# Optimization experiments

Hardware: AMD Instinct MI355X
Metric: run time of the kernel (lower is better)

The kernel has to match this reference:

```python
import jax, jax.numpy as jnp
import numpy as np

H = 32          # heads
E = 32          # head dim = mdl_channels // heads (must equal heads per module bug)
C = 1024        # mdl_channels == in_channels
MAXP = 128      # max_position_embeddings
EPS = 1e-5


def _layernorm(x, g, b):
    mu = jnp.mean(x, axis=-1, keepdims=True)
    var = jnp.var(x, axis=-1, keepdims=True)
    return (x - mu) * jax.lax.rsqrt(var + EPS) * g + b


def setup_inputs() -> dict:
    key = jax.random.key(0)
    ks = jax.random.split(key, 16)
    s = 0.02
    N, L = 4, 1024
    inp = {
        "x": jax.random.normal(ks[0], (N, L, C), jnp.float32),
        "Wq": jax.random.normal(ks[1], (C, C), jnp.float32) * s,
        "bq": jnp.zeros((C,), jnp.float32),
        "Wk": jax.random.normal(ks[2], (C, C), jnp.float32) * s,
        "bk": jnp.zeros((C,), jnp.float32),
        "Wv": jax.random.normal(ks[3], (C, C), jnp.float32) * s,
        "bv": jnp.zeros((C,), jnp.float32),
        "dist_emb": jax.random.normal(ks[4], (2 * MAXP + 1, E), jnp.float32) * s,
        "ln1_g": jnp.ones((C,), jnp.float32),
        "ln1_b": jnp.zeros((C,), jnp.float32),
        "ln2_g": jnp.ones((C,), jnp.float32),
        "ln2_b": jnp.zeros((C,), jnp.float32),
        "W1": jax.random.normal(ks[5], (C, C), jnp.float32) * s,
        "b1": jnp.zeros((C,), jnp.float32),
        "W2": jax.random.normal(ks[6], (C, C), jnp.float32) * s,
        "b2": jnp.zeros((C,), jnp.float32),
    }
    return inp


def reference(x, Wq, bq, Wk, bk, Wv, bv, dist_emb, ln1_g, ln1_b,
              ln2_g, ln2_b, W1, b1, W2, b2):
    N, L, _ = x.shape
    # QKV projections -> (N, L, H, E)
    q = (x @ Wq + bq).reshape(N, L, H, E)
    k = (x @ Wk + bk).reshape(N, L, H, E)
    v = (x @ Wv + bv).reshape(N, L, H, E)

    temp = 1.0 / np.sqrt(E).astype(np.float32)
    # content scores (N, H, L, S)
    QK = jnp.einsum('nlhe,nshe->nhls', q, k)
    # relative position scores (disentangled attention)
    pos = jnp.arange(L)
    dist = jnp.clip(pos[:, None] - pos[None, :], -MAXP, MAXP) + MAXP  # (L, L)
    pe = dist_emb[dist]                                              # (L, L, E)
    QK = QK + jnp.einsum('nlhe,lse->nhls', q, pe) \
            + jnp.einsum('nshe,lse->nhls', k, pe)
    A = jax.nn.softmax(temp * QK, axis=-1)          # dropout: eval mode (identity)
    t = jnp.einsum('nhls,nshe->nlhe', A, v).reshape(N, L, C)

    h = _layernorm(t + x, ln1_g, ln1_b)             # AddNorm (attention)
    m = jax.nn.relu(h @ W1 + b1) @ W2 + b2          # 2-layer MLP
    out = _layernorm(m + h, ln2_g, ln2_b)           # AddNorm (mlp)
    return jnp.swapaxes(out, 0, 1)                  # 'n f c -> f n c'
```

## Files before the change

kernel.cpp:

```cpp
#include <hip/hip_runtime.h>

#define H_ 32
#define E_ 32
#define C_ 1024
#define L_ 1024
#define N_ 4
#define M_ 4096
#define NH_ 128
#define D_ 257
#define DPAD 272
#define QDP 264
#define TEMP_ 0.17677669529663687f
#define QSCALE_ (TEMP_ * 1.4426950408889634f)

typedef unsigned short u16;
typedef __attribute__((ext_vector_type(8))) short short8;
typedef __attribute__((ext_vector_type(4))) float f32x4;
typedef __attribute__((ext_vector_type(4))) unsigned short u16x4;

__device__ __forceinline__ u16 f2bf(float f) {
  union { float f; unsigned u; } v; v.f = f;
  unsigned r = v.u + 0x7fffu + ((v.u >> 16) & 1u);
  return (u16)(r >> 16);
}
__device__ __forceinline__ float bf2f(u16 h) {
  union { unsigned u; float f; } v; v.u = ((unsigned)h) << 16;
  return v.f;
}
__device__ __forceinline__ f32x4 mfma16(short8 a, short8 b, f32x4 c) {
  return __builtin_amdgcn_mfma_f32_16x16x32_bf16(a, b, c, 0, 0, 0);
}
__device__ __forceinline__ float ex2(float x) {
#if __has_builtin(__builtin_amdgcn_exp2f)
  return __builtin_amdgcn_exp2f(x);
#else
  float r;
  asm("v_exp_f32 %0, %1\n\ts_nop 1" : "=v"(r) : "v"(x));
  return r;
#endif
}
__device__ __forceinline__ void gld16(const u16* g, u16* l) {
  __builtin_amdgcn_global_load_lds(
      (const __attribute__((address_space(1))) unsigned int*)g,
      (__attribute__((address_space(3))) unsigned int*)l, 16, 0, 0);
}

__global__ __launch_bounds__(256) void misc_kernel(
    const float* __restrict__ x, const float* __restrict__ demb,
    const float* __restrict__ bq, const float* __restrict__ bk,
    const float* __restrict__ bv, u16* __restrict__ xb,
    u16* __restrict__ demb_b, float* __restrict__ bqkv) {
  const int b = blockIdx.x, tid = threadIdx.x;
  if (b < 4096) {
    int i = b * 256 + tid;
    f32x4 v = reinterpret_cast<const f32x4*>(x)[i];
    u16x4 o2;
    o2[0] = f2bf(v[0]); o2[1] = f2bf(v[1]); o2[2] = f2bf(v[2]); o2[3] = f2bf(v[3]);
    reinterpret_cast<u16x4*>(xb)[i] = o2;
  } else {
    int i = (b - 4096) * 256 + tid;
    if (i < DPAD * E_) demb_b[i] = (i < D_ * E_) ? f2bf(demb[i]) : (u16)0;
    if (i < C_) { bqkv[i] = bq[i]; bqkv[C_ + i] = bk[i]; bqkv[2 * C_ + i] = bv[i]; }
  }
}

__global__ __launch_bounds__(256) void transpose_w_kernel(
    const float* __restrict__ Wq, const float* __restrict__ Wk,
    const float* __restrict__ Wv, const float* __restrict__ W1,
    const float* __restrict__ W2, u16* __restrict__ out_base) {
  __shared__ float tile[32][33];
  const int z = blockIdx.z;
  const float* in = (z == 0) ? Wq : (z == 1) ? Wk : (z == 2) ? Wv : (z == 3) ? W1 : W2;
  u16* out = out_base + (size_t)z * C_ * C_;
  int j0 = blockIdx.x * 32, c0 = blockIdx.y * 32;
#pragma unroll
  for (int i = 0; i < 4; ++i) {
    int cy = threadIdx.y + i * 8;
    tile[cy][threadIdx.x] = in[(size_t)(c0 + cy) * C_ + j0 + threadIdx.x];
  }
  __syncthreads();
#pragma unroll
  for (int i = 0; i < 4; ++i) {
    int jy = threadIdx.y + i * 8;
    out[(size_t)(j0 + jy) * C_ + c0 + threadIdx.x] = f2bf(tile[threadIdx.x][jy]);
  }
}

template <int EPI>
__global__ __launch_bounds__(256) void gemm128_kernel(
    const u16* __restrict__ A, const u16* __restrict__ Bt, int K,
    const float* __restrict__ bias,
    u16* __restrict__ out0, u16* __restrict__ out1, u16* __restrict__ out2) {
  __shared__ u16 As[128 * 64];
  __shared__ u16 Bs[128 * 64];
  const int bid = blockIdx.x;
  const int m0 = (bid & 31) << 7;
  const int n0 = (bid >> 5) << 7;
  const int tid = threadIdx.x;
  const int w = tid >> 6, lane = tid & 63, lhi = lane >> 4, llo = lane & 15;
  const int wr = w >> 1, wc = w & 1;
  const int w4 = w << 2;
  const int srow = lane >> 3, scol = (lane & 7) << 3;
  f32x4 acc[4][4] = {};
  for (int k0 = 0; k0 < K; k0 += 64) {
#pragma unroll
    for (int j = 0; j < 4; ++j) {
      const int seg = w4 + j;
      const int row = (seg << 3) + srow;
      gld16(&A[(size_t)(m0 + row) * K + k0 + scol], &As[seg << 9]);
      gld16(&Bt[(size_t)(n0 + row) * K + k0 + scol], &Bs[seg << 9]);
    }
    __syncthreads();
#pragma unroll
    for (int kk = 0; kk < 2; ++kk) {
      const int ko = (kk << 5) + lhi * 8;
      short8 af[4], bf[4];
#pragma unroll
      for (int mi = 0; mi < 4; ++mi)
        af[mi] = *reinterpret_cast<const short8*>(&As[(wr * 64 + mi * 16 + llo) * 64 + ko]);
#pragma unroll
      for (int ni = 0; ni < 4; ++ni)
        bf[ni] = *reinterpret_cast<const short8*>(&Bs[(wc * 64 + ni * 16 + llo) * 64 + ko]);
#pragma unroll
      for (int mi = 0; mi < 4; ++mi)
#pragma unroll
        for (int ni = 0; ni < 4; ++ni)
          acc[mi][ni] = mfma16(af[mi], bf[ni], acc[mi][ni]);
    }
    __syncthreads();
  }
#pragma unroll
  for (int mi = 0; mi < 4; ++mi)
#pragma unroll
    for (int ni = 0; ni < 4; ++ni)
#pragma unroll
      for (int r = 0; r < 4; ++r) {
        int row = m0 + wr * 64 + mi * 16 + lhi * 4 + r;
        int col = n0 + wc * 64 + ni * 16 + llo;
        float v = acc[mi][ni][r] + bias[col];
        if constexpr (EPI == 0) {
          int which = col >> 10, jj = col & 1023, h = jj >> 5, e2 = jj & 31;
          int n = row >> 10, l = row & 1023;
          int nh = (n << 5) | h;
          if (which == 0) v *= QSCALE_;
          u16 bvv = f2bf(v);
          if (which == 0)      out0[((size_t)((nh << 10) | l)) * 32 + e2] = bvv;
          else if (which == 1) out1[((size_t)((nh << 10) | l)) * 32 + e2] = bvv;
          else                 out2[(((size_t)(nh * 32 + e2)) << 10) | l] = bvv;
        } else if constexpr (EPI == 1) {
          out0[(size_t)row * C_ + col] = f2bf(fmaxf(v, 0.f));
        } else {
          out0[(size_t)row * C_ + col] = f2bf(v);
        }
      }
}

__global__ __launch_bounds__(256) void qdkd_kernel(
    const u16* __restrict__ src, const u16* __restrict__ demb,
    u16* __restrict__ dst, u16* __restrict__ aux0, u16* __restrict__ aux256) {
  const int wt = blockIdx.x * 4 + (threadIdx.x >> 6);
  const int lane = threadIdx.x & 63, lhi = lane >> 4, llo = lane & 15;
  const int m0 = wt << 4;
  short8 a = *reinterpret_cast<const short8*>(&src[(size_t)(m0 + llo) * E_ + lhi * 8]);
#pragma unroll
  for (int ct = 0; ct < 17; ++ct) {
    int d = ct * 16 + llo;
    short8 b = {0, 0, 0, 0, 0, 0, 0, 0};
    if (d < D_) b = *reinterpret_cast<const short8*>(&demb[d * E_ + lhi * 8]);
    f32x4 c = {};
    c = mfma16(a, b, c);
    if (d < D_) {
#pragma unroll
      for (int r = 0; r < 4; ++r) {
        u16 val = f2bf(c[r] * QSCALE_);
        dst[(size_t)(m0 + lhi * 4 + r) * D_ + d] = val;
        if (d == 0)   aux0[m0 + lhi * 4 + r] = val;
        if (d == 256) aux256[m0 + lhi * 4 + r] = val;
      }
    }
  }
}

__global__ __launch_bounds__(256) void attn_kernel(
    const u16* __restrict__ qw, const u16* __restrict__ kw,
    const u16* __restrict__ vT, const u16* __restrict__ dembp,
    const u16* __restrict__ KDg, const u16* __restrict__ kd0a,
    const u16* __restrict__ kd256a, u16* __restrict__ tb) {
  __shared__ u16 QDs[64 * QDP];
  __shared__ u16 kdc[2 * 1024];
  __shared__ u16 Pbuf[4 * 16 * 40];
  __shared__ float Lred[64];
  const int bid = blockIdx.x;
  const int nh = bid & (NH_ - 1);
  const int l0 = (bid >> 7) << 6;
  const int tid = threadIdx.x;
  const int w = tid >> 6, lane = tid & 63, lhi = lane >> 4, llo = lane & 15;
  const int lw0 = l0 + (w << 4);

  const u16* qb  = qw + (size_t)nh * (L_ * E_);
  const u16* kb  = kw + (size_t)nh * (L_ * E_);
  const u16* vb  = vT + (size_t)nh * (E_ * L_);
  const u16* kdg = KDg + (size_t)nh * ((size_t)L_ * D_);

  {
    const int side = tid >> 7, off = (tid & 127) * 8;
    const u16* srcA = (side ? kd256a : kd0a) + (size_t)nh * L_ + off;
    *reinterpret_cast<short8*>(&kdc[side * 1024 + off]) =
        *reinterpret_cast<const short8*>(srcA);
  }

  const short8 qA = *reinterpret_cast<const short8*>(&qb[(size_t)(lw0 + llo) * E_ + lhi * 8]);

#pragma unroll
  for (int dt = 0; dt < 17; ++dt) {
    short8 db = *reinterpret_cast<const short8*>(&dembp[(dt * 16 + llo) * E_ + lhi * 8]);
    f32x4 qd = {};
    qd = mfma16(qA, db, qd);
    const int qrow = (w << 4) + (lhi << 2);
#pragma unroll
    for (int r = 0; r < 4; ++r)
      QDs[(qrow + r) * QDP + dt * 16 + llo] = f2bf(qd[r]);
  }
  __syncthreads();

  const int qr4 = (w << 4) + (lhi << 2);
  float qdf0[4], qdf256[4];
#pragma unroll
  for (int r = 0; r < 4; ++r) {
    qdf0[r]   = bf2f(QDs[(qr4 + r) * QDP + 0]);
    qdf256[r] = bf2f(QDs[(qr4 + r) * QDP + 256]);
  }

  u16* Pw = &Pbuf[w * 16 * 40];
  f32x4 o0 = {}, o1 = {};
  float lacc[4] = {0.f, 0.f, 0.f, 0.f};

  for (int s0 = 0; s0 < L_; s0 += 32) {
    const int se = s0 + 2 * llo;
    short8 kB0 = *reinterpret_cast<const short8*>(&kb[(size_t)se * E_ + lhi * 8]);
    short8 kB1 = *reinterpret_cast<const short8*>(&kb[(size_t)(se + 1) * E_ + lhi * 8]);
    f32x4 st0 = {}, st1 = {};
    st0 = mfma16(qA, kB0, st0);
    st1 = mfma16(qA, kB1, st1);

    const int dmin = lw0 - s0 - 31, dmax = lw0 + 15 - s0;
    float p0[4], p1[4];
    if (dmin >= 128 || dmax <= -128) {
      const int sd = (dmin >= 128) ? 1 : 0;
      const float* qdf = sd ? qdf256 : qdf0;
      unsigned kc2 = *reinterpret_cast<const unsigned*>(&kdc[sd * 1024 + se]);
      const float kc0 = bf2f((u16)kc2), kc1 = bf2f((u16)(kc2 >> 16));
#pragma unroll
      for (int r = 0; r < 4; ++r) {
        p0[r] = ex2(st0[r] + qdf[r] + kc0);
        p1[r] = ex2(st1[r] + qdf[r] + kc1);
      }
    } else if (dmin >= -128 && dmax <= 128) {
      const int qoff = lw0 + (lhi << 2) + 128;
      u16x4 kd0v = *reinterpret_cast<const u16x4*>(&kdg[256 * se + qoff]);
      u16x4 kd1v = *reinterpret_cast<const u16x4*>(&kdg[256 * (se + 1) + qoff]);
#pragma unroll
      for (int r = 0; r < 4; ++r) {
        const int qq = lw0 + (lhi << 2) + r;
        float qd0 = bf2f(QDs[(qr4 + r) * QDP + (qq - se + 128)]);
        float qd1 = bf2f(QDs[(qr4 + r) * QDP + (qq - se + 127)]);
        p0[r] = ex2(st0[r] + qd0 + bf2f(kd0v[r]));
        p1[r] = ex2(st1[r] + qd1 + bf2f(kd1v[r]));
      }
    } else {
#pragma unroll
      for (int r = 0; r < 4; ++r) {
        const int qq = lw0 + (lhi << 2) + r;
        int d0 = qq - se;
        d0 = (d0 < -128 ? -128 : (d0 > 128 ? 128 : d0)) + 128;
        int d1 = qq - se - 1;
        d1 = (d1 < -128 ? -128 : (d1 > 128 ? 128 : d1)) + 128;
        float qd0 = bf2f(QDs[(qr4 + r) * QDP + d0]);
        float qd1 = bf2f(QDs[(qr4 + r) * QDP + d1]);
        float kd0 = bf2f(kdg[(size_t)se * D_ + d0]);
        float kd1 = bf2f(kdg[(size_t)(se + 1) * D_ + d1]);
        p0[r] = ex2(st0[r] + qd0 + kd0);
        p1[r] = ex2(st1[r] + qd1 + kd1);
      }
    }

#pragma unroll
    for (int r = 0; r < 4; ++r) {
      lacc[r] += p0[r] + p1[r];
      unsigned pw = (unsigned)f2bf(p0[r]) | ((unsigned)f2bf(p1[r]) << 16);
      *reinterpret_cast<unsigned*>(&Pw[((lhi << 2) + r) * 40 + 2 * llo]) = pw;
    }
    short8 pB = *reinterpret_cast<const short8*>(&Pw[llo * 40 + lhi * 8]);
    short8 vA0 = *reinterpret_cast<const short8*>(&vb[(size_t)llo * L_ + s0 + lhi * 8]);
    short8 vA1 = *reinterpret_cast<const short8*>(&vb[(size_t)(16 + llo) * L_ + s0 + lhi * 8]);
    o0 = mfma16(vA0, pB, o0);
    o1 = mfma16(vA1, pB, o1);
  }

#pragma unroll
  for (int r = 0; r < 4; ++r) {
    float t = lacc[r];
    t += __shfl_xor(t, 1); t += __shfl_xor(t, 2);
    t += __shfl_xor(t, 4); t += __shfl_xor(t, 8);
    if (llo == 0) Lred[(w << 4) + (lhi << 2) + r] = t;
  }
  const float inv = 1.0f / Lred[(w << 4) + llo];

  const int n = nh >> 5, h = nh & 31;
  const size_t obase = (((size_t)((n << 10) | (lw0 + llo))) * 32 + h) * 32;
  u16x4 w0, w1;
#pragma unroll
  for (int r = 0; r < 4; ++r) {
    w0[r] = f2bf(o0[r] * inv);
    w1[r] = f2bf(o1[r] * inv);
  }
  *reinterpret_cast<u16x4*>(&tb[obase + (lhi << 2)]) = w0;
  *reinterpret_cast<u16x4*>(&tb[obase + 16 + (lhi << 2)]) = w1;
}

__global__ __launch_bounds__(256) void ln1_kernel(
    const u16* __restrict__ tbuf, const float* __restrict__ x,
    const float* __restrict__ g, const float* __restrict__ b,
    u16* __restrict__ hb) {
  __shared__ float red[8];
  const int row = blockIdx.x, tid = threadIdx.x;
  const size_t base = (size_t)row * C_ + tid * 4;
  f32x4 xv = *reinterpret_cast<const f32x4*>(&x[base]);
  u16x4 tv = *reinterpret_cast<const u16x4*>(&tbuf[base]);
  float v[4]; float s1 = 0.f, s2 = 0.f;
#pragma unroll
  for (int i = 0; i < 4; ++i) {
    v[i] = xv[i] + bf2f(tv[i]);
    s1 += v[i]; s2 += v[i] * v[i];
  }
#pragma unroll
  for (int off = 32; off >= 1; off >>= 1) {
    s1 += __shfl_xor(s1, off); s2 += __shfl_xor(s2, off);
  }
  if ((tid & 63) == 0) { red[tid >> 6] = s1; red[4 + (tid >> 6)] = s2; }
  __syncthreads();
  float S1 = red[0] + red[1] + red[2] + red[3];
  float S2 = red[4] + red[5] + red[6] + red[7];
  float mu = S1 * (1.f / C_);
  float rs = rsqrtf(S2 * (1.f / C_) - mu * mu + 1e-5f);
#pragma unroll
  for (int i = 0; i < 4; ++i) {
    int c = tid * 4 + i;
    hb[base + i] = f2bf((v[i] - mu) * rs * g[c] + b[c]);
  }
}

__global__ __launch_bounds__(256) void ln2_kernel(
    const u16* __restrict__ mb, const u16* __restrict__ hb,
    const float* __restrict__ g, const float* __restrict__ b,
    float* __restrict__ out) {
  __shared__ float red[8];
  const int row = blockIdx.x, tid = threadIdx.x;
  const size_t base = (size_t)row * C_ + tid * 4;
  u16x4 mv = *reinterpret_cast<const u16x4*>(&mb[base]);
  u16x4 hv = *reinterpret_cast<const u16x4*>(&hb[base]);
  float v[4]; float s1 = 0.f, s2 = 0.f;
#pragma unroll
  for (int i = 0; i < 4; ++i) {
    v[i] = bf2f(mv[i]) + bf2f(hv[i]);
    s1 += v[i]; s2 += v[i] * v[i];
  }
#pragma unroll
  for (int off = 32; off >= 1; off >>= 1) {
    s1 += __shfl_xor(s1, off); s2 += __shfl_xor(s2, off);
  }
  if ((tid & 63) == 0) { red[tid >> 6] = s1; red[4 + (tid >> 6)] = s2; }
  __syncthreads();
  float S1 = red[0] + red[1] + red[2] + red[3];
  float S2 = red[4] + red[5] + red[6] + red[7];
  float mu = S1 * (1.f / C_);
  float rs = rsqrtf(S2 * (1.f / C_) - mu * mu + 1e-5f);
  const int n = row >> 10, l = row & 1023;
  const size_t ob = (size_t)(l * N_ + n) * C_ + tid * 4;
#pragma unroll
  for (int i = 0; i < 4; ++i) {
    int c = tid * 4 + i;
    out[ob + i] = (v[i] - mu) * rs * g[c] + b[c];
  }
}

extern "C" void kernel_launch(void* const* d_in, const int* in_sizes, int n_in,
                              void* d_out, int out_size, void* d_ws, size_t ws_size,
                              hipStream_t stream) {
  const float* x    = (const float*)d_in[0];
  const float* Wq   = (const float*)d_in[1];
  const float* bq   = (const float*)d_in[2];
  const float* Wk   = (const float*)d_in[3];
  const float* bk   = (const float*)d_in[4];
  const float* Wv   = (const float*)d_in[5];
  const float* bv   = (const float*)d_in[6];
  const float* demb = (const float*)d_in[7];
  const float* g1   = (const float*)d_in[8];
  const float* b1ln = (const float*)d_in[9];
  const float* g2   = (const float*)d_in[10];
  const float* b2ln = (const float*)d_in[11];
  const float* W1   = (const float*)d_in[12];
  const float* b1   = (const float*)d_in[13];
  const float* W2   = (const float*)d_in[14];
  const float* b2   = (const float*)d_in[15];
  float* outp = (float*)d_out;

  size_t o = 0;
  auto alloc = [&](size_t bytes) { size_t r = o; o += (bytes + 255) & ~(size_t)255; return r; };
  const size_t xb_o    = alloc((size_t)M_ * C_ * 2);
  const size_t wqkv_o  = alloc((size_t)3 * C_ * C_ * 2);
  const size_t w1_o    = alloc((size_t)C_ * C_ * 2);
  const size_t w2_o    = alloc((size_t)C_ * C_ * 2);
  const size_t bqkv_o  = alloc((size_t)3 * C_ * 4);
  const size_t demb_o  = alloc((size_t)DPAD * E_ * 2);
  const size_t q_o     = alloc((size_t)NH_ * L_ * E_ * 2);
  const size_t k_o     = alloc((size_t)NH_ * L_ * E_ * 2);
  const size_t vt_o    = alloc((size_t)NH_ * L_ * E_ * 2);
  const size_t kd_o    = alloc((size_t)NH_ * L_ * D_ * 2);
  const size_t kd0_o   = alloc((size_t)NH_ * L_ * 2);
  const size_t kd256_o = alloc((size_t)NH_ * L_ * 2);
  const size_t t_o     = alloc((size_t)M_ * C_ * 2);
  const size_t h_o     = alloc((size_t)M_ * C_ * 2);
  const size_t m1_o    = alloc((size_t)M_ * C_ * 2);
  const size_t m_o     = alloc((size_t)M_ * C_ * 2);
  if (o > ws_size) return;

  char* ws = (char*)d_ws;
  u16*   xb     = (u16*)(ws + xb_o);
  u16*   wqkv_t = (u16*)(ws + wqkv_o);
  u16*   w1_t   = (u16*)(ws + w1_o);
  u16*   w2_t   = (u16*)(ws + w2_o);
  float* bqkv   = (float*)(ws + bqkv_o);
  u16*   demb_b = (u16*)(ws + demb_o);
  u16*   q_ws   = (u16*)(ws + q_o);
  u16*   k_ws   = (u16*)(ws + k_o);
  u16*   vT_ws  = (u16*)(ws + vt_o);
  u16*   KD     = (u16*)(ws + kd_o);
  u16*   kd0a   = (u16*)(ws + kd0_o);
  u16*   kd256a = (u16*)(ws + kd256_o);
  u16*   t_b16  = (u16*)(ws + t_o);
  u16*   h_b16  = (u16*)(ws + h_o);
  u16*   m1_b16 = (u16*)(ws + m1_o);
  u16*   m_b16  = (u16*)(ws + m_o);

  misc_kernel<<<4096 + 34, 256, 0, stream>>>(x, demb, bq, bk, bv, xb, demb_b, bqkv);
  dim3 tb_(32, 8), tg_(32, 32, 5);
  transpose_w_kernel<<<tg_, tb_, 0, stream>>>(Wq, Wk, Wv, W1, W2, wqkv_t);

  gemm128_kernel<0><<<32 * 24, 256, 0, stream>>>(xb, wqkv_t, C_, bqkv, q_ws, k_ws, vT_ws);

  qdkd_kernel<<<2048, 256, 0, stream>>>(k_ws, demb_b, KD, kd0a, kd256a);

  attn_kernel<<<NH_ * 16, 256, 0, stream>>>(q_ws, k_ws, vT_ws, demb_b, KD, kd0a, kd256a, t_b16);

  ln1_kernel<<<M_, 256, 0, stream>>>(t_b16, x, g1, b1ln, h_b16);

  gemm128_kernel<1><<<32 * 8, 256, 0, stream>>>(h_b16, w1_t, C_, b1, m1_b16, nullptr, nullptr);
  gemm128_kernel<2><<<32 * 8, 256, 0, stream>>>(m1_b16, w2_t, C_, b2, m_b16, nullptr, nullptr);

  ln2_kernel<<<M_, 256, 0, stream>>>(m_b16, h_b16, g2, b2ln, outp);
}
```

Before: 311.8 us.

## Shrink attention LDS, drop block sync, and retune band branch thresholds

```diff
diff --git a/kernel.cpp b/kernel.cpp
--- a/kernel.cpp
+++ b/kernel.cpp
@@ -9,7 +9,6 @@
 #define NH_ 128
 #define D_ 257
 #define DPAD 272
-#define QDP 264
 #define TEMP_ 0.17677669529663687f
 #define QSCALE_ (TEMP_ * 1.4426950408889634f)
 
@@ -165,8 +164,7 @@
 #pragma unroll
   for (int ct = 0; ct < 17; ++ct) {
     int d = ct * 16 + llo;
-    short8 b = {0, 0, 0, 0, 0, 0, 0, 0};
-    if (d < D_) b = *reinterpret_cast<const short8*>(&demb[d * E_ + lhi * 8]);
+    short8 b = *reinterpret_cast<const short8*>(&demb[d * E_ + lhi * 8]);
     f32x4 c = {};
     c = mfma16(a, b, c);
     if (d < D_) {
@@ -181,13 +179,12 @@
   }
 }
 
-__global__ __launch_bounds__(256) void attn_kernel(
+__global__ __launch_bounds__(256, 4) void attn_kernel(
     const u16* __restrict__ qw, const u16* __restrict__ kw,
     const u16* __restrict__ vT, const u16* __restrict__ dembp,
     const u16* __restrict__ KDg, const u16* __restrict__ kd0a,
     const u16* __restrict__ kd256a, u16* __restrict__ tb) {
-  __shared__ u16 QDs[64 * QDP];
-  __shared__ u16 kdc[2 * 1024];
+  __shared__ u16 QDs[64 * 257];
   __shared__ u16 Pbuf[4 * 16 * 40];
   __shared__ float Lred[64];
   const int bid = blockIdx.x;
@@ -196,103 +193,101 @@
   const int tid = threadIdx.x;
   const int w = tid >> 6, lane = tid & 63, lhi = lane >> 4, llo = lane & 15;
   const int lw0 = l0 + (w << 4);
+  const int lg = lw0 + llo;
 
   const u16* qb  = qw + (size_t)nh * (L_ * E_);
   const u16* kb  = kw + (size_t)nh * (L_ * E_);
   const u16* vb  = vT + (size_t)nh * (E_ * L_);
   const u16* kdg = KDg + (size_t)nh * ((size_t)L_ * D_);
-
-  {
-    const int side = tid >> 7, off = (tid & 127) * 8;
-    const u16* srcA = (side ? kd256a : kd0a) + (size_t)nh * L_ + off;
-    *reinterpret_cast<short8*>(&kdc[side * 1024 + off]) =
-        *reinterpret_cast<const short8*>(srcA);
-  }
-
-  const short8 qA = *reinterpret_cast<const short8*>(&qb[(size_t)(lw0 + llo) * E_ + lhi * 8]);
+  const u16* k0g = kd0a + (size_t)nh * L_;
+  const u16* k2g = kd256a + (size_t)nh * L_;
+
+  const short8 qA = *(const short8*)&qb[(size_t)lg * E_ + lhi * 8];
+  const int qr4 = (w << 4) + (lhi << 2);
 
 #pragma unroll
   for (int dt = 0; dt < 17; ++dt) {
-    short8 db = *reinterpret_cast<const short8*>(&dembp[(dt * 16 + llo) * E_ + lhi * 8]);
+    const int col = dt * 16 + llo;
+    short8 db = *(const short8*)&dembp[col * E_ + lhi * 8];
     f32x4 qd = {};
     qd = mfma16(qA, db, qd);
-    const int qrow = (w << 4) + (lhi << 2);
-#pragma unroll
-    for (int r = 0; r < 4; ++r)
-      QDs[(qrow + r) * QDP + dt * 16 + llo] = f2bf(qd[r]);
-  }
-  __syncthreads();
-
-  const int qr4 = (w << 4) + (lhi << 2);
+    if (col < 257) {
+#pragma unroll
+      for (int r = 0; r < 4; ++r)
+        QDs[(qr4 + r) * 257 + col] = f2bf(qd[r]);
+    }
+  }
   float qdf0[4], qdf256[4];
 #pragma unroll
   for (int r = 0; r < 4; ++r) {
-    qdf0[r]   = bf2f(QDs[(qr4 + r) * QDP + 0]);
-    qdf256[r] = bf2f(QDs[(qr4 + r) * QDP + 256]);
-  }
-
-  u16* Pw = &Pbuf[w * 16 * 40];
+    qdf0[r]   = bf2f(QDs[(qr4 + r) * 257 + 0]);
+    qdf256[r] = bf2f(QDs[(qr4 + r) * 257 + 256]);
+  }
+
   f32x4 o0 = {}, o1 = {};
   float lacc[4] = {0.f, 0.f, 0.f, 0.f};
+  u16* Pw = &Pbuf[w * 16 * 40];
 
   for (int s0 = 0; s0 < L_; s0 += 32) {
     const int se = s0 + 2 * llo;
-    short8 kB0 = *reinterpret_cast<const short8*>(&kb[(size_t)se * E_ + lhi * 8]);
-    short8 kB1 = *reinterpret_cast<const short8*>(&kb[(size_t)(se + 1) * E_ + lhi * 8]);
+    short8 kB0 = *(const short8*)&kb[(size_t)se * E_ + lhi * 8];
+    short8 kB1 = *(const short8*)&kb[(size_t)(se + 1) * E_ + lhi * 8];
     f32x4 st0 = {}, st1 = {};
     st0 = mfma16(qA, kB0, st0);
     st1 = mfma16(qA, kB1, st1);
 
-    const int dmin = lw0 - s0 - 31, dmax = lw0 + 15 - s0;
     float p0[4], p1[4];
-    if (dmin >= 128 || dmax <= -128) {
-      const int sd = (dmin >= 128) ? 1 : 0;
-      const float* qdf = sd ? qdf256 : qdf0;
-      unsigned kc2 = *reinterpret_cast<const unsigned*>(&kdc[sd * 1024 + se]);
-      const float kc0 = bf2f((u16)kc2), kc1 = bf2f((u16)(kc2 >> 16));
+    const int delta = lw0 - s0;
+    if (delta >= 159 || delta <= -143) {
+      const bool fh = delta >= 159;
+      const float* qdf = fh ? qdf256 : qdf0;
+      const u16* kcg = fh ? k2g : k0g;
+      unsigned kc2 = *(const unsigned*)&kcg[se];
+      const float kf0 = bf2f((u16)kc2), kf1 = bf2f((u16)(kc2 >> 16));
 #pragma unroll
       for (int r = 0; r < 4; ++r) {
-        p0[r] = ex2(st0[r] + qdf[r] + kc0);
-        p1[r] = ex2(st1[r] + qdf[r] + kc1);
+        p0[r] = ex2(st0[r] + qdf[r] + kf0);
+        p1[r] = ex2(st1[r] + qdf[r] + kf1);
       }
-    } else if (dmin >= -128 && dmax <= 128) {
-      const int qoff = lw0 + (lhi << 2) + 128;
-      u16x4 kd0v = *reinterpret_cast<const u16x4*>(&kdg[256 * se + qoff]);
-      u16x4 kd1v = *reinterpret_cast<const u16x4*>(&kdg[256 * (se + 1) + qoff]);
+    } else if (delta >= -97 && delta <= 113) {
+      const int fb = (se << 8) + lw0 + (lhi << 2) + 128;
+      u16x4 kv0 = *(const u16x4*)&kdg[fb];
+      u16x4 kv1 = *(const u16x4*)&kdg[fb + 256];
+      const int dq = lw0 + (lhi << 2) - se + 128;
 #pragma unroll
       for (int r = 0; r < 4; ++r) {
-        const int qq = lw0 + (lhi << 2) + r;
-        float qd0 = bf2f(QDs[(qr4 + r) * QDP + (qq - se + 128)]);
-        float qd1 = bf2f(QDs[(qr4 + r) * QDP + (qq - se + 127)]);
-        p0[r] = ex2(st0[r] + qd0 + bf2f(kd0v[r]));
-        p1[r] = ex2(st1[r] + qd1 + bf2f(kd1v[r]));
+        float qd0 = bf2f(QDs[(qr4 + r) * 257 + dq + r]);
+        float qd1 = bf2f(QDs[(qr4 + r) * 257 + dq + r - 1]);
+        p0[r] = ex2(st0[r] + qd0 + bf2f(kv0[r]));
+        p1[r] = ex2(st1[r] + qd1 + bf2f(kv1[r]));
       }
     } else {
+      const int rb0 = se * D_, rb1 = rb0 + D_;
 #pragma unroll
       for (int r = 0; r < 4; ++r) {
-        const int qq = lw0 + (lhi << 2) + r;
-        int d0 = qq - se;
-        d0 = (d0 < -128 ? -128 : (d0 > 128 ? 128 : d0)) + 128;
-        int d1 = qq - se - 1;
-        d1 = (d1 < -128 ? -128 : (d1 > 128 ? 128 : d1)) + 128;
-        float qd0 = bf2f(QDs[(qr4 + r) * QDP + d0]);
-        float qd1 = bf2f(QDs[(qr4 + r) * QDP + d1]);
-        float kd0 = bf2f(kdg[(size_t)se * D_ + d0]);
-        float kd1 = bf2f(kdg[(size_t)(se + 1) * D_ + d1]);
-        p0[r] = ex2(st0[r] + qd0 + kd0);
-        p1[r] = ex2(st1[r] + qd1 + kd1);
+        const int q = lw0 + (lhi << 2) + r;
+        int d0 = q - se + 128;
+        d0 = d0 < 0 ? 0 : (d0 > 256 ? 256 : d0);
+        int d1 = q - se + 127;
+        d1 = d1 < 0 ? 0 : (d1 > 256 ? 256 : d1);
+        float qd0 = bf2f(QDs[(qr4 + r) * 257 + d0]);
+        float qd1 = bf2f(QDs[(qr4 + r) * 257 + d1]);
+        p0[r] = ex2(st0[r] + qd0 + bf2f(kdg[rb0 + d0]));
+        p1[r] = ex2(st1[r] + qd1 + bf2f(kdg[rb1 + d1]));
       }
     }
 
 #pragma unroll
     for (int r = 0; r < 4; ++r) {
       lacc[r] += p0[r] + p1[r];
-      unsigned pw = (unsigned)f2bf(p0[r]) | ((unsigned)f2bf(p1[r]) << 16);
+      union { float f; unsigned u; } a0, a1;
+      a0.f = p0[r]; a1.f = p1[r];
+      unsigned pw = ((a0.u + 0x8000u) >> 16) | ((a1.u + 0x8000u) & 0xffff0000u);
       *reinterpret_cast<unsigned*>(&Pw[((lhi << 2) + r) * 40 + 2 * llo]) = pw;
     }
-    short8 pB = *reinterpret_cast<const short8*>(&Pw[llo * 40 + lhi * 8]);
-    short8 vA0 = *reinterpret_cast<const short8*>(&vb[(size_t)llo * L_ + s0 + lhi * 8]);
-    short8 vA1 = *reinterpret_cast<const short8*>(&vb[(size_t)(16 + llo) * L_ + s0 + lhi * 8]);
+    short8 pB = *(const short8*)&Pw[llo * 40 + lhi * 8];
+    short8 vA0 = *(const short8*)&vb[(size_t)llo * L_ + s0 + lhi * 8];
+    short8 vA1 = *(const short8*)&vb[(size_t)(16 + llo) * L_ + s0 + lhi * 8];
     o0 = mfma16(vA0, pB, o0);
     o1 = mfma16(vA1, pB, o1);
   }
@@ -307,7 +302,7 @@
   const float inv = 1.0f / Lred[(w << 4) + llo];
 
   const int n = nh >> 5, h = nh & 31;
-  const size_t obase = (((size_t)((n << 10) | (lw0 + llo))) * 32 + h) * 32;
+  const size_t obase = (((size_t)((n << 10) | lg)) * 32 + h) * 32;
   u16x4 w0, w1;
 #pragma unroll
   for (int r = 0; r < 4; ++r) {
```

Result: faster. 298.4 us (-4.3%).
